# Performance work log

Measured on AMD Instinct MI355X. Metric: run time of the kernel, lower is better.

Reference implementation:

```python
import jax, jax.numpy as jnp
import numpy as np

NUM_HEADS = 16
D_MODEL = 1024
DEPTH = D_MODEL // NUM_HEADS


def rope_sincos(seq_len, depth):
    # standard RoPE: inv_freq over even dims, sin/cos tiled to full depth
    inv_freq = 1.0 / (10000.0 ** (jnp.arange(0, depth, 2, dtype=jnp.float32) / depth))
    ang = jnp.arange(seq_len, dtype=jnp.float32)[:, None] * inv_freq[None, :]  # [S, depth/2]
    sin = jnp.concatenate([jnp.sin(ang), jnp.sin(ang)], axis=-1)  # [S, depth]
    cos = jnp.concatenate([jnp.cos(ang), jnp.cos(ang)], axis=-1)
    return sin, cos


def apply_rope(x, sin, cos):
    # x: [B,H,S,depth]; rotate-half formulation
    half = x.shape[-1] // 2
    x1, x2 = x[..., :half], x[..., half:]
    rot = jnp.concatenate([-x2, x1], axis=-1)
    return x * cos + rot * sin


def setup_inputs() -> dict:
    key = jax.random.key(0)
    ks = jax.random.split(key, 5)
    s = 1.0 / np.sqrt(D_MODEL)
    return {
        "x": jax.random.normal(ks[0], (2, 2048, D_MODEL), dtype=jnp.float32),
        "wq": jax.random.normal(ks[1], (D_MODEL, D_MODEL), dtype=jnp.float32) * s,
        "bq": jnp.zeros((D_MODEL,), jnp.float32),
        "wk": jax.random.normal(ks[2], (D_MODEL, D_MODEL), dtype=jnp.float32) * s,
        "bk": jnp.zeros((D_MODEL,), jnp.float32),
        "wv": jax.random.normal(ks[3], (D_MODEL, D_MODEL), dtype=jnp.float32) * s,
        "bv": jnp.zeros((D_MODEL,), jnp.float32),
        "wo": jax.random.normal(ks[4], (D_MODEL, D_MODEL), dtype=jnp.float32) * s,
        "bo": jnp.zeros((D_MODEL,), jnp.float32),
    }


def reference(x, wq, bq, wk, bk, wv, bv, wo, bo):
    B, S, _ = x.shape

    def split_heads(t):  # [B,S,D] -> [B,H,S,depth]
        return t.reshape(B, S, NUM_HEADS, DEPTH).transpose(0, 2, 1, 3)

    Q = split_heads(x @ wq + bq)
    K = split_heads(x @ wk + bk)
    V = split_heads(x @ wv + bv)

    sin, cos = rope_sincos(S, DEPTH)  # [S, depth], broadcasts over B,H
    Q = apply_rope(Q, sin, cos)
    K = apply_rope(K, sin, cos)

    scores = jnp.einsum("bhqd,bhkd->bhqk", Q, K) / jnp.sqrt(jnp.float32(DEPTH))
    weights = jax.nn.softmax(scores, axis=-1)
    out = jnp.einsum("bhqk,bhkd->bhqd", weights, V)
    out = out.transpose(0, 2, 1, 3).reshape(B, S, D_MODEL)
    return out @ wo + bo
```

## Files before the change

kernel.cpp:

```cpp
#include <hip/hip_runtime.h>

#define DM 1024
#define SEQ 2048
#define NH 16
#define DH 64
#define BATCH 2

typedef _Float16 half_t;
typedef _Float16 half8 __attribute__((ext_vector_type(8)));
typedef _Float16 half4 __attribute__((ext_vector_type(4)));
typedef float f32x4 __attribute__((ext_vector_type(4)));

__device__ __forceinline__ f32x4 mfma16(half8 a, half8 b, f32x4 c) {
  return __builtin_amdgcn_mfma_f32_16x16x32_f16(a, b, c, 0, 0, 0);
}

__device__ __forceinline__ void gl2lds16(const half_t* g, half_t* l) {
  __builtin_amdgcn_global_load_lds((const __attribute__((address_space(1))) void*)g,
                                   (__attribute__((address_space(3))) void*)l, 16, 0, 0);
}


__global__ void cvt_x_kernel(const float* __restrict__ x, half_t* __restrict__ xh) {
  int i = (blockIdx.x * 256 + threadIdx.x) * 4;
  float4 v = *(const float4*)(x + i);
  half4 h = { (half_t)v.x, (half_t)v.y, (half_t)v.z, (half_t)v.w };
  *(half4*)(xh + i) = h;
}

__global__ void wtrans_kernel(const float* __restrict__ w0, const float* __restrict__ w1,
                              const float* __restrict__ w2, const float* __restrict__ w3,
                              half_t* __restrict__ o0, half_t* __restrict__ o1,
                              half_t* __restrict__ o2, half_t* __restrict__ o3) {
  __shared__ float tile[32][33];
  const float* w = (blockIdx.z == 0) ? w0 : (blockIdx.z == 1) ? w1 : (blockIdx.z == 2) ? w2 : w3;
  half_t* o = (blockIdx.z == 0) ? o0 : (blockIdx.z == 1) ? o1 : (blockIdx.z == 2) ? o2 : o3;
  int tx = threadIdx.x, ty0 = threadIdx.y;
  int bx = blockIdx.x * 32, by = blockIdx.y * 32;
#pragma unroll
  for (int i = 0; i < 4; i++) {
    int ty = ty0 + i * 8;
    tile[ty][tx] = w[(size_t)(by + ty) * DM + bx + tx];
  }
  __syncthreads();
#pragma unroll
  for (int i = 0; i < 4; i++) {
    int ty = ty0 + i * 8;
    o[(size_t)(bx + ty) * DM + by + tx] = (half_t)tile[tx][ty];
  }
}

__global__ void ropetab_kernel(float* __restrict__ st, float* __restrict__ ct) {
  int idx = blockIdx.x * 256 + threadIdx.x;
  int s = idx >> 5, i = idx & 31;
  float freq = exp2f(-(float)i * (13.287712379549449f / 32.0f));
  float ang = (float)s * freq;
  st[idx] = sinf(ang);
  ct[idx] = cosf(ang);
}


__global__ __launch_bounds__(256)
void qkv_kernel(const half_t* __restrict__ xh,
                const half_t* __restrict__ wtq, const half_t* __restrict__ wtk,
                const half_t* __restrict__ wtv,
                const float* __restrict__ bq, const float* __restrict__ bk,
                const float* __restrict__ bv,
                const float* __restrict__ st, const float* __restrict__ ctab,
                half_t* __restrict__ Qh, half_t* __restrict__ Kh, half_t* __restrict__ Vt) {
  const int tid = threadIdx.x;
  const int wid = tid >> 6, lane = tid & 63;
  const int l16 = lane & 15, quad = lane >> 4;
  const int m0 = blockIdx.y * 128, n0 = blockIdx.x * 128;
  const int g = blockIdx.z;
  const half_t* wt = (g == 0) ? wtq : (g == 1) ? wtk : wtv;
  const float* bias = (g == 0) ? bq : (g == 1) ? bk : bv;
  __shared__ __align__(16) half_t As[128 * 40];
  __shared__ __align__(16) half_t Bs[128 * 40];
  f32x4 acc[4][4] = {};
  const int wrow = (wid >> 1) * 64, wcol = (wid & 1) * 64;

  for (int k0 = 0; k0 < DM; k0 += 32) {
#pragma unroll
    for (int i = 0; i < 2; i++) {
      int cc = tid + i * 256;
      int row = cc >> 2, col8 = (cc & 3) * 8;
      *(half8*)&As[row * 40 + col8] = *(const half8*)&xh[(size_t)(m0 + row) * DM + k0 + col8];
      *(half8*)&Bs[row * 40 + col8] = *(const half8*)&wt[(size_t)(n0 + row) * DM + k0 + col8];
    }
    __syncthreads();
    half8 a[4], b[4];
#pragma unroll
    for (int rt = 0; rt < 4; rt++) a[rt] = *(const half8*)&As[(wrow + rt * 16 + l16) * 40 + quad * 8];
#pragma unroll
    for (int ct = 0; ct < 4; ct++) b[ct] = *(const half8*)&Bs[(wcol + ct * 16 + l16) * 40 + quad * 8];
#pragma unroll
    for (int rt = 0; rt < 4; rt++)
#pragma unroll
      for (int ct = 0; ct < 4; ct++)
        acc[rt][ct] = mfma16(a[rt], b[ct], acc[rt][ct]);
    __syncthreads();
  }

  const int h = (n0 + wcol) >> 6;
  const float qscale = 0.125f * 1.44269504089f;
  float bv4[4];
#pragma unroll
  for (int ct = 0; ct < 4; ct++) bv4[ct] = bias[n0 + wcol + ct * 16 + l16];
#pragma unroll
  for (int rt = 0; rt < 4; rt++) {
#pragma unroll
    for (int r = 0; r < 4; r++) {
      int m = m0 + wrow + rt * 16 + quad * 4 + r;
      int bb = m >> 11, s = m & 2047;
      float v0 = acc[rt][0][r] + bv4[0];
      float v1 = acc[rt][1][r] + bv4[1];
      float v2 = acc[rt][2][r] + bv4[2];
      float v3 = acc[rt][3][r] + bv4[3];
      if (g == 2) {
        size_t vb = ((size_t)(bb * NH + h)) * DH;
        Vt[(vb + l16) * SEQ + s]      = (half_t)v0;
        Vt[(vb + 16 + l16) * SEQ + s] = (half_t)v1;
        Vt[(vb + 32 + l16) * SEQ + s] = (half_t)v2;
        Vt[(vb + 48 + l16) * SEQ + s] = (half_t)v3;
      } else {
        float sn0 = st[s * 32 + l16], cs0 = ctab[s * 32 + l16];
        float sn1 = st[s * 32 + 16 + l16], cs1 = ctab[s * 32 + 16 + l16];
        float o0 = v0 * cs0 - v2 * sn0;
        float o1 = v1 * cs1 - v3 * sn1;
        float o2 = v2 * cs0 + v0 * sn0;
        float o3 = v3 * cs1 + v1 * sn1;
        if (g == 0) { o0 *= qscale; o1 *= qscale; o2 *= qscale; o3 *= qscale; }
        half_t* dst = (g == 0) ? Qh : Kh;
        size_t base = ((size_t)(bb * NH + h) * SEQ + s) * DH;
        dst[base + l16]      = (half_t)o0;
        dst[base + 16 + l16] = (half_t)o1;
        dst[base + 32 + l16] = (half_t)o2;
        dst[base + 48 + l16] = (half_t)o3;
      }
    }
  }
}


__global__ __launch_bounds__(256)
void attn_kernel(const half_t* __restrict__ Qh, const half_t* __restrict__ Kh,
                 const half_t* __restrict__ Vt, half_t* __restrict__ AO) {
  const int tid = threadIdx.x;
  const int wid = tid >> 6, lane = tid & 63;
  const int l16 = lane & 15, quad = lane >> 4;
  const int bh = blockIdx.y;
  const int bb = bh >> 4, h = bh & 15;
  const int q0 = blockIdx.x * 64 + wid * 16;
  const half_t* Q = Qh + (size_t)bh * SEQ * DH;
  const half_t* K = Kh + (size_t)bh * SEQ * DH;
  const half_t* V = Vt + (size_t)bh * DH * SEQ;
  __shared__ __align__(16) half_t Ks[64 * 64];
  __shared__ __align__(16) half_t Vs[64 * 64];
  __shared__ __align__(16) half_t pbuf[4][16 * 72];
  half_t* myp = pbuf[wid];

  const int r0 = tid >> 3,        c0 = (tid & 7) ^ (r0 & 7);
  const int r1 = (tid + 256) >> 3, c1 = (tid & 7) ^ (r1 & 7);
  const int sw0 = ((quad ^ (l16 & 7)) * 8);
  const int sw1 = (((quad + 4) ^ (l16 & 7)) * 8);

  half8 aq0 = *(const half8*)&Q[(size_t)(q0 + l16) * DH + quad * 8];
  half8 aq1 = *(const half8*)&Q[(size_t)(q0 + l16) * DH + 32 + quad * 8];
  f32x4 o[4] = {};
  float lrow[4] = {0.f, 0.f, 0.f, 0.f};
  const f32x4 cinit = {-12.f, -12.f, -12.f, -12.f};

  for (int kb0 = 0; kb0 < SEQ; kb0 += 64) {
    __syncthreads();
    gl2lds16(&K[(size_t)(kb0 + r0) * DH + c0 * 8], &Ks[tid * 8]);
    gl2lds16(&K[(size_t)(kb0 + r1) * DH + c1 * 8], &Ks[(tid + 256) * 8]);
    gl2lds16(&V[(size_t)r0 * SEQ + kb0 + c0 * 8], &Vs[tid * 8]);
    gl2lds16(&V[(size_t)r1 * SEQ + kb0 + c1 * 8], &Vs[(tid + 256) * 8]);
    __syncthreads();

    f32x4 sf[4];
#pragma unroll
    for (int kt = 0; kt < 4; kt++) {
      const half_t* krow = &Ks[(kt * 16 + l16) * 64];
      half8 b0 = *(const half8*)&krow[sw0];
      half8 b1 = *(const half8*)&krow[sw1];
      f32x4 z = cinit;
      z = mfma16(aq0, b0, z);
      z = mfma16(aq1, b1, z);
      sf[kt] = z;
    }
#pragma unroll
    for (int kt = 0; kt < 4; kt++)
#pragma unroll
      for (int r = 0; r < 4; r++) {
        float p = __builtin_amdgcn_exp2f(sf[kt][r]);
        lrow[r] += p;
        myp[(quad * 4 + r) * 72 + kt * 16 + l16] = (half_t)p;
      }
    half8 ap0 = *(const half8*)&myp[l16 * 72 + quad * 8];
    half8 ap1 = *(const half8*)&myp[l16 * 72 + 32 + quad * 8];
#pragma unroll
    for (int dt = 0; dt < 4; dt++) {
      const half_t* vrow = &Vs[(dt * 16 + l16) * 64];
      half8 bv0 = *(const half8*)&vrow[sw0];
      half8 bv1 = *(const half8*)&vrow[sw1];
      o[dt] = mfma16(ap0, bv0, o[dt]);
      o[dt] = mfma16(ap1, bv1, o[dt]);
    }
  }
#pragma unroll
  for (int d = 1; d <= 8; d <<= 1)
#pragma unroll
    for (int r = 0; r < 4; r++)
      lrow[r] += __shfl_xor(lrow[r], d);
#pragma unroll
  for (int r = 0; r < 4; r++) lrow[r] = 1.f / lrow[r];
#pragma unroll
  for (int dt = 0; dt < 4; dt++)
#pragma unroll
    for (int r = 0; r < 4; r++) {
      int srow = q0 + quad * 4 + r;
      AO[((size_t)bb * SEQ + srow) * DM + h * DH + dt * 16 + l16] = (half_t)(o[dt][r] * lrow[r]);
    }
}


__global__ __launch_bounds__(256)
void out_kernel(const half_t* __restrict__ AO, const half_t* __restrict__ wto,
                const float* __restrict__ bo, float* __restrict__ out) {
  const int tid = threadIdx.x;
  const int wid = tid >> 6, lane = tid & 63;
  const int l16 = lane & 15, quad = lane >> 4;
  const int m0 = blockIdx.y * 128, n0 = blockIdx.x * 128;
  __shared__ __align__(16) half_t As[128 * 40];
  __shared__ __align__(16) half_t Bs[128 * 40];
  f32x4 acc[4][4] = {};
  const int wrow = (wid >> 1) * 64, wcol = (wid & 1) * 64;

  for (int k0 = 0; k0 < DM; k0 += 32) {
#pragma unroll
    for (int i = 0; i < 2; i++) {
      int cc = tid + i * 256;
      int row = cc >> 2, col8 = (cc & 3) * 8;
      *(half8*)&As[row * 40 + col8] = *(const half8*)&AO[(size_t)(m0 + row) * DM + k0 + col8];
      *(half8*)&Bs[row * 40 + col8] = *(const half8*)&wto[(size_t)(n0 + row) * DM + k0 + col8];
    }
    __syncthreads();
    half8 a[4], b[4];
#pragma unroll
    for (int rt = 0; rt < 4; rt++) a[rt] = *(const half8*)&As[(wrow + rt * 16 + l16) * 40 + quad * 8];
#pragma unroll
    for (int ct = 0; ct < 4; ct++) b[ct] = *(const half8*)&Bs[(wcol + ct * 16 + l16) * 40 + quad * 8];
#pragma unroll
    for (int rt = 0; rt < 4; rt++)
#pragma unroll
      for (int ct = 0; ct < 4; ct++)
        acc[rt][ct] = mfma16(a[rt], b[ct], acc[rt][ct]);
    __syncthreads();
  }
  float bv4[4];
#pragma unroll
  for (int ct = 0; ct < 4; ct++) bv4[ct] = bo[n0 + wcol + ct * 16 + l16];
#pragma unroll
  for (int rt = 0; rt < 4; rt++)
#pragma unroll
    for (int r = 0; r < 4; r++) {
      int m = m0 + wrow + rt * 16 + quad * 4 + r;
#pragma unroll
      for (int ct = 0; ct < 4; ct++)
        out[(size_t)m * DM + n0 + wcol + ct * 16 + l16] = acc[rt][ct][r] + bv4[ct];
    }
}


extern "C" void kernel_launch(void* const* d_in, const int* in_sizes, int n_in,
                              void* d_out, int out_size, void* d_ws, size_t ws_size,
                              hipStream_t stream) {
  (void)in_sizes; (void)n_in; (void)out_size; (void)ws_size;
  const float* x  = (const float*)d_in[0];
  const float* wq = (const float*)d_in[1];
  const float* bq = (const float*)d_in[2];
  const float* wk = (const float*)d_in[3];
  const float* bk = (const float*)d_in[4];
  const float* wv = (const float*)d_in[5];
  const float* bv = (const float*)d_in[6];
  const float* wo = (const float*)d_in[7];
  const float* bo = (const float*)d_in[8];
  char* ws = (char*)d_ws;
  const size_t MB = 1u << 20;
  half_t* xh  = (half_t*)(ws + 0);
  half_t* wtq = (half_t*)(ws + 8 * MB);
  half_t* wtk = (half_t*)(ws + 10 * MB);
  half_t* wtv = (half_t*)(ws + 12 * MB);
  half_t* wto = (half_t*)(ws + 14 * MB);
  float*  st  = (float*)(ws + 16 * MB);
  float*  ctb = (float*)(ws + 16 * MB + 256 * 1024);
  half_t* Qh  = (half_t*)(ws + 17 * MB);
  half_t* Kh  = (half_t*)(ws + 25 * MB);
  half_t* Vt  = (half_t*)(ws + 33 * MB);
  half_t* AO  = (half_t*)(ws + 41 * MB);
  float* out = (float*)d_out;

  cvt_x_kernel<<<4096, 256, 0, stream>>>(x, xh);
  wtrans_kernel<<<dim3(32, 32, 4), dim3(32, 8), 0, stream>>>(wq, wk, wv, wo, wtq, wtk, wtv, wto);
  ropetab_kernel<<<256, 256, 0, stream>>>(st, ctb);
  qkv_kernel<<<dim3(8, 32, 3), 256, 0, stream>>>(xh, wtq, wtk, wtv, bq, bk, bv, st, ctb, Qh, Kh, Vt);
  attn_kernel<<<dim3(32, 32), 256, 0, stream>>>(Qh, Kh, Vt, AO);
  out_kernel<<<dim3(8, 32), 256, 0, stream>>>(AO, wto, bo, out);
}
```

Before: 225.2 us.

## Use direct global-to-LDS loads in GEMMs, split V transpose, shrink out-proj tile

Both projection GEMMs now stage A and B tiles into LDS with global_load_lds and an XOR-swizzled, unpadded layout in place of register-staged padded copies. The trailing barrier is dropped in favour of one at the top of each iteration. The QKV kernel writes V in row-major head layout, and a separate transpose kernel produces the V^T layout the attention kernel needs. This replaces the strided scalar scatter writes of the old epilogue. The output projection uses 128x64 tiles to double the block count, and AO reuses the xh workspace region, at the cost of an extra kernel launch and an extra pass over V.

Measured after the change: 212.7 us. 1.06x faster.

```diff
diff --git a/kernel.cpp b/kernel.cpp
--- a/kernel.cpp
+++ b/kernel.cpp
@@ -59,6 +59,32 @@
   ct[idx] = cosf(ang);
 }
 
+__global__ __launch_bounds__(256)
+void vtrans_kernel(const half_t* __restrict__ Vh, half_t* __restrict__ Vt) {
+  __shared__ half_t t[64 * 72];
+  const int tid = threadIdx.x;
+  const int bh = blockIdx.y;
+  const int s0 = blockIdx.x * 64;
+  const half_t* src = Vh + (size_t)bh * SEQ * DH + (size_t)s0 * DH;
+  half_t* dst = Vt + (size_t)bh * DH * SEQ;
+#pragma unroll
+  for (int i = 0; i < 2; i++) {
+    int s = tid + i * 256;
+    int row = s >> 3, blk = s & 7;
+    *(half8*)&t[row * 72 + blk * 8] = *(const half8*)&src[(size_t)row * DH + blk * 8];
+  }
+  __syncthreads();
+  const int d = tid >> 2;
+#pragma unroll
+  for (int i = 0; i < 2; i++) {
+    int sb = (tid & 3) * 8 + i * 32;
+    half8 v;
+#pragma unroll
+    for (int j = 0; j < 8; j++) v[j] = t[(sb + j) * 72 + d];
+    *(half8*)&dst[(size_t)d * SEQ + s0 + sb] = v;
+  }
+}
+
 
 __global__ __launch_bounds__(256)
 void qkv_kernel(const half_t* __restrict__ xh,
@@ -67,7 +93,7 @@
                 const float* __restrict__ bq, const float* __restrict__ bk,
                 const float* __restrict__ bv,
                 const float* __restrict__ st, const float* __restrict__ ctab,
-                half_t* __restrict__ Qh, half_t* __restrict__ Kh, half_t* __restrict__ Vt) {
+                half_t* __restrict__ Qh, half_t* __restrict__ Kh, half_t* __restrict__ Vh) {
   const int tid = threadIdx.x;
   const int wid = tid >> 6, lane = tid & 63;
   const int l16 = lane & 15, quad = lane >> 4;
@@ -75,35 +101,39 @@
   const int g = blockIdx.z;
   const half_t* wt = (g == 0) ? wtq : (g == 1) ? wtk : wtv;
   const float* bias = (g == 0) ? bq : (g == 1) ? bk : bv;
-  __shared__ __align__(16) half_t As[128 * 40];
-  __shared__ __align__(16) half_t Bs[128 * 40];
+  __shared__ __align__(16) half_t As[128 * 32];
+  __shared__ __align__(16) half_t Bs[128 * 32];
   f32x4 acc[4][4] = {};
   const int wrow = (wid >> 1) * 64, wcol = (wid & 1) * 64;
 
+  const int ar0 = tid >> 2,          ab0 = (tid & 3) ^ ((ar0 >> 1) & 3);
+  const int ar1 = (tid + 256) >> 2,  ab1 = (tid & 3) ^ ((ar1 >> 1) & 3);
+  const int swz = (l16 >> 1) & 3;
+
   for (int k0 = 0; k0 < DM; k0 += 32) {
-#pragma unroll
-    for (int i = 0; i < 2; i++) {
-      int cc = tid + i * 256;
-      int row = cc >> 2, col8 = (cc & 3) * 8;
-      *(half8*)&As[row * 40 + col8] = *(const half8*)&xh[(size_t)(m0 + row) * DM + k0 + col8];
-      *(half8*)&Bs[row * 40 + col8] = *(const half8*)&wt[(size_t)(n0 + row) * DM + k0 + col8];
-    }
+    __syncthreads();
+    gl2lds16(&xh[(size_t)(m0 + ar0) * DM + k0 + ab0 * 8], &As[tid * 8]);
+    gl2lds16(&xh[(size_t)(m0 + ar1) * DM + k0 + ab1 * 8], &As[(tid + 256) * 8]);
+    gl2lds16(&wt[(size_t)(n0 + ar0) * DM + k0 + ab0 * 8], &Bs[tid * 8]);
+    gl2lds16(&wt[(size_t)(n0 + ar1) * DM + k0 + ab1 * 8], &Bs[(tid + 256) * 8]);
     __syncthreads();
     half8 a[4], b[4];
 #pragma unroll
-    for (int rt = 0; rt < 4; rt++) a[rt] = *(const half8*)&As[(wrow + rt * 16 + l16) * 40 + quad * 8];
-#pragma unroll
-    for (int ct = 0; ct < 4; ct++) b[ct] = *(const half8*)&Bs[(wcol + ct * 16 + l16) * 40 + quad * 8];
+    for (int rt = 0; rt < 4; rt++)
+      a[rt] = *(const half8*)&As[((wrow + rt * 16 + l16) * 4 + (quad ^ swz)) * 8];
+#pragma unroll
+    for (int ct = 0; ct < 4; ct++)
+      b[ct] = *(const half8*)&Bs[((wcol + ct * 16 + l16) * 4 + (quad ^ swz)) * 8];
 #pragma unroll
     for (int rt = 0; rt < 4; rt++)
 #pragma unroll
       for (int ct = 0; ct < 4; ct++)
         acc[rt][ct] = mfma16(a[rt], b[ct], acc[rt][ct]);
-    __syncthreads();
   }
 
   const int h = (n0 + wcol) >> 6;
   const float qscale = 0.125f * 1.44269504089f;
+  half_t* dst = (g == 0) ? Qh : (g == 1) ? Kh : Vh;
   float bv4[4];
 #pragma unroll
   for (int ct = 0; ct < 4; ct++) bv4[ct] = bias[n0 + wcol + ct * 16 + l16];
@@ -117,27 +147,21 @@
       float v1 = acc[rt][1][r] + bv4[1];
       float v2 = acc[rt][2][r] + bv4[2];
       float v3 = acc[rt][3][r] + bv4[3];
-      if (g == 2) {
-        size_t vb = ((size_t)(bb * NH + h)) * DH;
-        Vt[(vb + l16) * SEQ + s]      = (half_t)v0;
-        Vt[(vb + 16 + l16) * SEQ + s] = (half_t)v1;
-        Vt[(vb + 32 + l16) * SEQ + s] = (half_t)v2;
-        Vt[(vb + 48 + l16) * SEQ + s] = (half_t)v3;
-      } else {
+      float o0 = v0, o1 = v1, o2 = v2, o3 = v3;
+      if (g != 2) {
         float sn0 = st[s * 32 + l16], cs0 = ctab[s * 32 + l16];
         float sn1 = st[s * 32 + 16 + l16], cs1 = ctab[s * 32 + 16 + l16];
-        float o0 = v0 * cs0 - v2 * sn0;
-        float o1 = v1 * cs1 - v3 * sn1;
-        float o2 = v2 * cs0 + v0 * sn0;
-        float o3 = v3 * cs1 + v1 * sn1;
+        o0 = v0 * cs0 - v2 * sn0;
+        o1 = v1 * cs1 - v3 * sn1;
+        o2 = v2 * cs0 + v0 * sn0;
+        o3 = v3 * cs1 + v1 * sn1;
         if (g == 0) { o0 *= qscale; o1 *= qscale; o2 *= qscale; o3 *= qscale; }
-        half_t* dst = (g == 0) ? Qh : Kh;
-        size_t base = ((size_t)(bb * NH + h) * SEQ + s) * DH;
-        dst[base + l16]      = (half_t)o0;
-        dst[base + 16 + l16] = (half_t)o1;
-        dst[base + 32 + l16] = (half_t)o2;
-        dst[base + 48 + l16] = (half_t)o3;
       }
+      size_t base = ((size_t)(bb * NH + h) * SEQ + s) * DH;
+      dst[base + l16]      = (half_t)o0;
+      dst[base + 16 + l16] = (half_t)o1;
+      dst[base + 32 + l16] = (half_t)o2;
+      dst[base + 48 + l16] = (half_t)o3;
     }
   }
 }
@@ -160,7 +184,7 @@
   __shared__ __align__(16) half_t pbuf[4][16 * 72];
   half_t* myp = pbuf[wid];
 
-  const int r0 = tid >> 3,        c0 = (tid & 7) ^ (r0 & 7);
+  const int r0 = tid >> 3,         c0 = (tid & 7) ^ (r0 & 7);
   const int r1 = (tid + 256) >> 3, c1 = (tid & 7) ^ (r1 & 7);
   const int sw0 = ((quad ^ (l16 & 7)) * 8);
   const int sw1 = (((quad + 4) ^ (l16 & 7)) * 8);
@@ -232,44 +256,46 @@
   const int tid = threadIdx.x;
   const int wid = tid >> 6, lane = tid & 63;
   const int l16 = lane & 15, quad = lane >> 4;
-  const int m0 = blockIdx.y * 128, n0 = blockIdx.x * 128;
-  __shared__ __align__(16) half_t As[128 * 40];
-  __shared__ __align__(16) half_t Bs[128 * 40];
-  f32x4 acc[4][4] = {};
-  const int wrow = (wid >> 1) * 64, wcol = (wid & 1) * 64;
+  const int m0 = blockIdx.y * 128, n0 = blockIdx.x * 64;
+  __shared__ __align__(16) half_t As[128 * 32];
+  __shared__ __align__(16) half_t Bs[64 * 32];
+  f32x4 acc[4][2] = {};
+  const int wrow = (wid >> 1) * 64, wcol = (wid & 1) * 32;
+
+  const int ar0 = tid >> 2,         ab0 = (tid & 3) ^ ((ar0 >> 1) & 3);
+  const int ar1 = (tid + 256) >> 2, ab1 = (tid & 3) ^ ((ar1 >> 1) & 3);
+  const int swz = (l16 >> 1) & 3;
 
   for (int k0 = 0; k0 < DM; k0 += 32) {
-#pragma unroll
-    for (int i = 0; i < 2; i++) {
-      int cc = tid + i * 256;
-      int row = cc >> 2, col8 = (cc & 3) * 8;
-      *(half8*)&As[row * 40 + col8] = *(const half8*)&AO[(size_t)(m0 + row) * DM + k0 + col8];
-      *(half8*)&Bs[row * 40 + col8] = *(const half8*)&wto[(size_t)(n0 + row) * DM + k0 + col8];
-    }
-    __syncthreads();
-    half8 a[4], b[4];
-#pragma unroll
-    for (int rt = 0; rt < 4; rt++) a[rt] = *(const half8*)&As[(wrow + rt * 16 + l16) * 40 + quad * 8];
-#pragma unroll
-    for (int ct = 0; ct < 4; ct++) b[ct] = *(const half8*)&Bs[(wcol + ct * 16 + l16) * 40 + quad * 8];
+    __syncthreads();
+    gl2lds16(&AO[(size_t)(m0 + ar0) * DM + k0 + ab0 * 8], &As[tid * 8]);
+    gl2lds16(&AO[(size_t)(m0 + ar1) * DM + k0 + ab1 * 8], &As[(tid + 256) * 8]);
+    gl2lds16(&wto[(size_t)(n0 + ar0) * DM + k0 + ab0 * 8], &Bs[tid * 8]);
+    __syncthreads();
+    half8 a[4], b[2];
 #pragma unroll
     for (int rt = 0; rt < 4; rt++)
-#pragma unroll
-      for (int ct = 0; ct < 4; ct++)
+      a[rt] = *(const half8*)&As[((wrow + rt * 16 + l16) * 4 + (quad ^ swz)) * 8];
+#pragma unroll
+    for (int ct = 0; ct < 2; ct++)
+      b[ct] = *(const half8*)&Bs[((wcol + ct * 16 + l16) * 4 + (quad ^ swz)) * 8];
+#pragma unroll
+    for (int rt = 0; rt < 4; rt++)
+#pragma unroll
+      for (int ct = 0; ct < 2; ct++)
         acc[rt][ct] = mfma16(a[rt], b[ct], acc[rt][ct]);
-    __syncthreads();
-  }
-  float bv4[4];
-#pragma unroll
-  for (int ct = 0; ct < 4; ct++) bv4[ct] = bo[n0 + wcol + ct * 16 + l16];
+  }
+  float bv2[2];
+#pragma unroll
+  for (int ct = 0; ct < 2; ct++) bv2[ct] = bo[n0 + wcol + ct * 16 + l16];
 #pragma unroll
   for (int rt = 0; rt < 4; rt++)
 #pragma unroll
     for (int r = 0; r < 4; r++) {
       int m = m0 + wrow + rt * 16 + quad * 4 + r;
 #pragma unroll
-      for (int ct = 0; ct < 4; ct++)
-        out[(size_t)m * DM + n0 + wcol + ct * 16 + l16] = acc[rt][ct][r] + bv4[ct];
+      for (int ct = 0; ct < 2; ct++)
+        out[(size_t)m * DM + n0 + wcol + ct * 16 + l16] = acc[rt][ct][r] + bv2[ct];
     }
 }
 
@@ -290,6 +316,7 @@
   char* ws = (char*)d_ws;
   const size_t MB = 1u << 20;
   half_t* xh  = (half_t*)(ws + 0);
+  half_t* AO  = (half_t*)(ws + 0);
   half_t* wtq = (half_t*)(ws + 8 * MB);
   half_t* wtk = (half_t*)(ws + 10 * MB);
   half_t* wtv = (half_t*)(ws + 12 * MB);
@@ -298,14 +325,15 @@
   float*  ctb = (float*)(ws + 16 * MB + 256 * 1024);
   half_t* Qh  = (half_t*)(ws + 17 * MB);
   half_t* Kh  = (half_t*)(ws + 25 * MB);
-  half_t* Vt  = (half_t*)(ws + 33 * MB);
-  half_t* AO  = (half_t*)(ws + 41 * MB);
+  half_t* Vh  = (half_t*)(ws + 33 * MB);
+  half_t* Vt  = (half_t*)(ws + 41 * MB);
   float* out = (float*)d_out;
 
   cvt_x_kernel<<<4096, 256, 0, stream>>>(x, xh);
   wtrans_kernel<<<dim3(32, 32, 4), dim3(32, 8), 0, stream>>>(wq, wk, wv, wo, wtq, wtk, wtv, wto);
   ropetab_kernel<<<256, 256, 0, stream>>>(st, ctb);
-  qkv_kernel<<<dim3(8, 32, 3), 256, 0, stream>>>(xh, wtq, wtk, wtv, bq, bk, bv, st, ctb, Qh, Kh, Vt);
+  qkv_kernel<<<dim3(8, 32, 3), 256, 0, stream>>>(xh, wtq, wtk, wtv, bq, bk, bv, st, ctb, Qh, Kh, Vh);
+  vtrans_kernel<<<dim3(32, 32), 256, 0, stream>>>(Vh, Vt);
   attn_kernel<<<dim3(32, 32), 256, 0, stream>>>(Qh, Kh, Vt, AO);
-  out_kernel<<<dim3(8, 32), 256, 0, stream>>>(AO, wto, bo, out);
-}
+  out_kernel<<<dim3(16, 32), 256, 0, stream>>>(AO, wto, bo, out);
+}
```
